# Performance work log

Hardware: AMD Instinct MI355X
Metric: run time of the kernel (lower is better)

## Reference

```python
import jax, jax.numpy as jnp
import numpy as np

B, D, UD = 32, 1024, 256          # batch, chunks_dim, units_dim
ENT, NENT = 32, 64                # entity_size, n_entities
S, C = NENT * ENT, NENT + 1       # src_len (units), n_chunks
NEG_INF = float('-inf')


def setup_inputs() -> dict:
    key = jax.random.key(0)
    ks = jax.random.split(key, 9)
    source = jax.random.normal(ks[0], (B, D), jnp.float32)
    high_level_repr = jax.random.normal(ks[1], (C, B, D), jnp.float32)
    pos_embs = jax.random.normal(ks[2], (S, B, UD), jnp.float32)
    low_level_repr = jax.random.normal(ks[3], (S, B, D), jnp.float32)
    low_level_mask = jax.random.randint(ks[4], (NENT, B, ENT), 0, 2).astype(bool)
    high_level_mask = jax.random.randint(ks[5], (1, B, C), 0, 2).astype(bool)
    high_level_mask = high_level_mask.at[..., 0].set(False)  # avoid all-masked chunk softmax
    W_unit = jax.random.normal(ks[6], (UD, D), jnp.float32) / np.sqrt(D)
    W_chunk = jax.random.normal(ks[7], (D, D), jnp.float32) / np.sqrt(D)
    W_out = jax.random.normal(ks[8], (D, 2 * D), jnp.float32) / np.sqrt(2 * D)
    return {"source": source, "high_level_repr": high_level_repr, "pos_embs": pos_embs,
            "low_level_repr": low_level_repr, "low_level_mask": low_level_mask,
            "high_level_mask": high_level_mask, "W_unit": W_unit, "W_chunk": W_chunk,
            "W_out": W_out}


def reference(source, high_level_repr, pos_embs, low_level_repr,
              low_level_mask, high_level_mask, W_unit, W_chunk, W_out):
    # batch-first views (torch transposes(0,1))
    hl = jnp.swapaxes(high_level_repr, 0, 1)    # (B, C, D)
    ll = jnp.swapaxes(low_level_repr, 0, 1)     # (B, S, D)
    pe = jnp.swapaxes(pos_embs, 0, 1)           # (B, S, UD)
    ll_mask = jnp.swapaxes(low_level_mask, 0, 1)   # (B, NENT, ENT)
    hl_mask = jnp.swapaxes(high_level_mask, 0, 1)  # (B, 1, C)

    # 'general' attention scorers, tgt_len == 1
    q_u = source @ W_unit.T                      # (B, UD)
    align_units = jnp.einsum('bd,bsd->bs', q_u, pe)        # (B, S)
    q_c = source @ W_chunk.T                     # (B, D)
    align_chunks = jnp.einsum('bd,bcd->bc', q_c, hl)[:, None, :]  # (B, 1, C)

    # low-level masked softmax per entity, NaN rows -> 0
    au = align_units.reshape(B, NENT, ENT)
    au = jnp.where(ll_mask, NEG_INF, au)
    au = jax.nn.softmax(au, axis=-1)
    all_masked = jnp.all(ll_mask, axis=-1)       # (B, NENT) rows that were NaN
    au = jnp.where(all_masked[..., None], 0.0, au)
    au = au.reshape(B, 1, S)

    # high-level masked softmax, drop chunk 0, inflate to unit granularity
    ac = jnp.where(hl_mask, NEG_INF, align_chunks)
    ac = jax.nn.softmax(ac, axis=-1)[:, :, 1:]   # (B, 1, C-1)
    ac_inflated = jnp.repeat(ac, ENT, axis=-1)   # (B, 1, S)

    align_vectors = ac_inflated * au             # (B, 1, S)
    c = jnp.einsum('bts,bsd->btd', align_vectors, ll)  # (B, 1, D)
    concat = jnp.concatenate([c, source[:, None, :]], axis=-1).reshape(B, 2 * D)
    attn_h = jnp.tanh(concat @ W_out.T)          # (B, D); tanh since attn_type='general'

    return (attn_h,
            align_vectors[:, 0, :],              # (B, S)
            ac[:, 0, :],                         # (B, C-1)
            au.reshape(B, S))                    # (B, S)
```

## Files before the change

### kernel.cpp

```cpp
#include <hip/hip_runtime.h>

#define B 32
#define D 1024
#define UD 256
#define ENT 32
#define NENT 64
#define S 2048
#define C 65

__device__ __forceinline__ float dot4(float4 w, const float* q) {
    return w.x * q[0] + w.y * q[1] + w.z * q[2] + w.w * q[3];
}

__global__ __launch_bounds__(256) void k_proj(const float* __restrict__ src,
                                              const float* __restrict__ Wu,
                                              const float* __restrict__ Wc,
                                              float* __restrict__ qu,
                                              float* __restrict__ qc) {
    __shared__ alignas(16) float s_src[4][D];
    __shared__ float red[4][64][4];
    int t = threadIdx.x, rg = blockIdx.x, bg = blockIdx.y;
    for (int f = t; f < 4 * (D / 4); f += 256) {
        int bb = f >> 8, i4 = f & 255;
        float4 v = *(const float4*)(src + (size_t)(bg * 4 + bb) * D + i4 * 4);
        *(float4*)(&s_src[bb][i4 * 4]) = v;
    }
    __syncthreads();
    int jl = t & 63, kq = t >> 6;
    int gj = rg * 64 + jl;
    const float* wrow = (gj < UD) ? (Wu + (size_t)gj * D) : (Wc + (size_t)(gj - UD) * D);
    const float4* wp = (const float4*)wrow + kq * 64;
    float acc[4] = {0.f, 0.f, 0.f, 0.f};
#pragma unroll 4
    for (int i = 0; i < 64; ++i) {
        float4 w = wp[i];
        int k = kq * 256 + i * 4;
#pragma unroll
        for (int bb = 0; bb < 4; ++bb) acc[bb] += dot4(w, &s_src[bb][k]);
    }
#pragma unroll
    for (int bb = 0; bb < 4; ++bb) red[kq][jl][bb] = acc[bb];
    __syncthreads();
    {
        int jl2 = t & 63, bb = t >> 6;
        float s = red[0][jl2][bb] + red[1][jl2][bb] + red[2][jl2][bb] + red[3][jl2][bb];
        int gj2 = rg * 64 + jl2, b = bg * 4 + bb;
        if (gj2 < UD) qu[b * UD + gj2] = s;
        else qc[b * D + (gj2 - UD)] = s;
    }
}

__global__ __launch_bounds__(256) void k_units(const float* __restrict__ pe,
                                               const int* __restrict__ lmask,
                                               const float* __restrict__ qu,
                                               float* __restrict__ out_au) {
    __shared__ alignas(16) float q[UD];
    __shared__ float part[256];
    int n = blockIdx.x, b = blockIdx.y, t = threadIdx.x;
    q[t] = qu[b * UD + t];
    __syncthreads();
    int e = t >> 3, r = t & 7;
    const float4* pp = (const float4*)(pe + (size_t)(n * ENT + e) * B * UD + (size_t)b * UD) + r * 8;
    float acc = 0.f;
#pragma unroll
    for (int i = 0; i < 8; ++i) acc += dot4(pp[i], &q[(r * 8 + i) * 4]);
    part[t] = acc;
    __syncthreads();
    if (t < ENT) {
        float sc = 0.f;
#pragma unroll
        for (int r2 = 0; r2 < 8; ++r2) sc += part[t * 8 + r2];
        bool m = lmask[(size_t)n * B * ENT + b * ENT + t] != 0;
        float v = m ? -1e30f : sc;
        float mx = v;
        for (int o = 16; o >= 1; o >>= 1) mx = fmaxf(mx, __shfl_xor(mx, o));
        float p = m ? 0.f : __expf(v - mx);
        float sm = p;
        for (int o = 16; o >= 1; o >>= 1) sm += __shfl_xor(sm, o);
        out_au[b * S + n * ENT + t] = (sm > 0.f) ? (p / sm) : 0.f;
    }
}

__global__ __launch_bounds__(256) void k_chunks(const float* __restrict__ hl,
                                                const int* __restrict__ hmask,
                                                const float* __restrict__ qc,
                                                float* __restrict__ out_ac) {
    __shared__ alignas(16) float q[D];
    __shared__ float sc[C];
    __shared__ float red[2];
    int b = blockIdx.x, t = threadIdx.x;
    for (int i = t; i < D / 4; i += 256)
        *(float4*)(&q[i * 4]) = *(const float4*)(qc + (size_t)b * D + i * 4);
    __syncthreads();
    int w = t >> 6, l = t & 63;
    for (int c = w; c < C; c += 4) {
        const float4* hp = (const float4*)(hl + (size_t)(c * B + b) * D);
        float acc = 0.f;
#pragma unroll
        for (int i = 0; i < 4; ++i) {
            int f = l + 64 * i;
            float4 h = hp[f];
            acc += dot4(h, &q[f * 4]);
        }
        for (int o = 32; o >= 1; o >>= 1) acc += __shfl_xor(acc, o);
        if (l == 0) sc[c] = acc;
    }
    __syncthreads();
    if (t == 0) {
        float mx = -1e30f;
        for (int c = 0; c < C; ++c) {
            float v = hmask[b * C + c] ? -1e30f : sc[c];
            mx = fmaxf(mx, v);
        }
        float sm = 0.f;
        for (int c = 0; c < C; ++c) {
            float v = hmask[b * C + c] ? -1e30f : sc[c];
            sm += __expf(v - mx);
        }
        red[0] = mx;
        red[1] = sm;
    }
    __syncthreads();
    if (t >= 1 && t < C) {
        bool m = hmask[b * C + t] != 0;
        float p = m ? 0.f : __expf(sc[t] - red[0]) / red[1];
        out_ac[b * NENT + (t - 1)] = p;
    }
}

__global__ __launch_bounds__(256) void k_ctx(const float* __restrict__ ll,
                                             const float* __restrict__ out_au,
                                             const float* __restrict__ out_ac,
                                             float* __restrict__ pf,
                                             float* __restrict__ out_av) {
    __shared__ float s_av[256];
    int ss = blockIdx.x, b = blockIdx.y, t = threadIdx.x;
    {
        int s = ss * 256 + t;
        int n = s >> 5;
        float a = out_ac[b * NENT + n] * out_au[b * S + s];
        s_av[t] = a;
        out_av[b * S + s] = a;
    }
    __syncthreads();
    float4 acc = {0.f, 0.f, 0.f, 0.f};
    const float4* base = (const float4*)(ll + (size_t)(ss * 256) * B * D + (size_t)b * D) + t;
#pragma unroll 8
    for (int j = 0; j < 256; ++j) {
        float4 x = base[(size_t)j * (B * D / 4)];
        float wv = s_av[j];
        acc.x += wv * x.x;
        acc.y += wv * x.y;
        acc.z += wv * x.z;
        acc.w += wv * x.w;
    }
    *(float4*)(pf + (size_t)ss * B * D + (size_t)b * D + t * 4) = acc;
}

__global__ __launch_bounds__(256) void k_red(const float* __restrict__ pf,
                                             float* __restrict__ cf) {
    int f = blockIdx.x * 256 + threadIdx.x;
    float s = 0.f;
#pragma unroll
    for (int ss = 0; ss < 8; ++ss) s += pf[(size_t)ss * B * D + f];
    cf[f] = s;
}

__global__ __launch_bounds__(256) void k_out(const float* __restrict__ Wo,
                                             const float* __restrict__ src,
                                             const float* __restrict__ cf,
                                             float* __restrict__ out_h) {
    __shared__ alignas(16) float cc[4][2 * D];
    __shared__ float red[4][64][4];
    int t = threadIdx.x, jg = blockIdx.x, bg = blockIdx.y;
    for (int f = t; f < 4 * (2 * D / 4); f += 256) {
        int bb = f >> 9, part = f & 511;
        int b = bg * 4 + bb;
        float4 v;
        if (part < 256) v = *(const float4*)(cf + (size_t)b * D + part * 4);
        else v = *(const float4*)(src + (size_t)b * D + (part - 256) * 4);
        *(float4*)(&cc[bb][part * 4]) = v;
    }
    __syncthreads();
    int jl = t & 63, kq = t >> 6;
    int j = jg * 64 + jl;
    const float4* wp = (const float4*)(Wo + (size_t)j * 2 * D) + kq * 128;
    float acc[4] = {0.f, 0.f, 0.f, 0.f};
#pragma unroll 4
    for (int i = 0; i < 128; ++i) {
        float4 w = wp[i];
        int k = kq * 512 + i * 4;
#pragma unroll
        for (int bb = 0; bb < 4; ++bb) acc[bb] += dot4(w, &cc[bb][k]);
    }
#pragma unroll
    for (int bb = 0; bb < 4; ++bb) red[kq][jl][bb] = acc[bb];
    __syncthreads();
    {
        int jl2 = t & 63, bb = t >> 6;
        float s = red[0][jl2][bb] + red[1][jl2][bb] + red[2][jl2][bb] + red[3][jl2][bb];
        out_h[(size_t)(bg * 4 + bb) * D + jg * 64 + jl2] = tanhf(s);
    }
}

extern "C" void kernel_launch(void* const* d_in, const int* in_sizes, int n_in,
                              void* d_out, int out_size, void* d_ws, size_t ws_size,
                              hipStream_t stream) {
    const float* src = (const float*)d_in[0];
    const float* hl = (const float*)d_in[1];
    const float* pe = (const float*)d_in[2];
    const float* ll = (const float*)d_in[3];
    const int* lmask = (const int*)d_in[4];
    const int* hmask = (const int*)d_in[5];
    const float* Wu = (const float*)d_in[6];
    const float* Wc = (const float*)d_in[7];
    const float* Wo = (const float*)d_in[8];

    float* out = (float*)d_out;
    float* out_h = out;
    float* out_av = out + B * D;
    float* out_ac = out_av + B * S;
    float* out_au = out_ac + B * NENT;

    float* ws = (float*)d_ws;
    float* qu = ws;
    float* qc = qu + B * UD;
    float* cf = qc + B * D;
    float* pf = cf + B * D;

    k_proj<<<dim3(20, 8), 256, 0, stream>>>(src, Wu, Wc, qu, qc);
    k_units<<<dim3(NENT, B), 256, 0, stream>>>(pe, lmask, qu, out_au);
    k_chunks<<<dim3(B), 256, 0, stream>>>(hl, hmask, qc, out_ac);
    k_ctx<<<dim3(8, B), 256, 0, stream>>>(ll, out_au, out_ac, pf, out_av);
    k_red<<<dim3(B * D / 256), 256, 0, stream>>>(pf, cf);
    k_out<<<dim3(16, 8), 256, 0, stream>>>(Wo, src, cf, out_h);
}
```

Before: 478.2 us.

## Fuse unit scoring, softmaxes and context reduction into one kernel; parallelize chunk scores

Chunk scores move into a new kernel with one block per (chunk, batch), which raises parallelism over the old 32-block chunk kernel. Unit scoring, the per-entity softmax, the chunk softmax and the weighted context sum now run in one 512-thread kernel per (slab, batch). Inside that kernel the context loop is split into two halves that are combined through shared memory. The separate slab-reduction kernel is dropped and its work folded into k_out's load phase. This removes launches and global round trips of intermediates, but the fused kernel still has only 256 blocks and each one recomputes the chunk softmax.

```diff
diff --git a/kernel.cpp b/kernel.cpp
--- a/kernel.cpp
+++ b/kernel.cpp
@@ -7,6 +7,8 @@
 #define NENT 64
 #define S 2048
 #define C 65
+#define NSLAB 8
+#define SROWS 256
 
 __device__ __forceinline__ float dot4(float4 w, const float* q) {
     return w.x * q[0] + w.y * q[1] + w.z * q[2] + w.w * q[3];
@@ -50,125 +52,121 @@
     }
 }
 
-__global__ __launch_bounds__(256) void k_units(const float* __restrict__ pe,
+__global__ __launch_bounds__(256) void k_score(const float* __restrict__ hl,
+                                               const float* __restrict__ qc,
+                                               float* __restrict__ sc) {
+    __shared__ float red[4];
+    int c = blockIdx.x, b = blockIdx.y, t = threadIdx.x;
+    const float4* hp = (const float4*)(hl + ((size_t)c * B + b) * D);
+    const float4* qp = (const float4*)(qc + (size_t)b * D);
+    float4 h = hp[t];
+    float4 q = qp[t];
+    float acc = h.x * q.x + h.y * q.y + h.z * q.z + h.w * q.w;
+    for (int o = 32; o >= 1; o >>= 1) acc += __shfl_xor(acc, o);
+    if ((t & 63) == 0) red[t >> 6] = acc;
+    __syncthreads();
+    if (t == 0) sc[b * C + c] = red[0] + red[1] + red[2] + red[3];
+}
+
+__global__ __launch_bounds__(512) void k_fused(const float* __restrict__ pe,
+                                               const float* __restrict__ ll,
                                                const int* __restrict__ lmask,
+                                               const int* __restrict__ hmask,
                                                const float* __restrict__ qu,
-                                               float* __restrict__ out_au) {
+                                               const float* __restrict__ sc,
+                                               float* __restrict__ pf,
+                                               float* __restrict__ out_au,
+                                               float* __restrict__ out_ac,
+                                               float* __restrict__ out_av) {
     __shared__ alignas(16) float q[UD];
-    __shared__ float part[256];
-    int n = blockIdx.x, b = blockIdx.y, t = threadIdx.x;
-    q[t] = qu[b * UD + t];
-    __syncthreads();
-    int e = t >> 3, r = t & 7;
-    const float4* pp = (const float4*)(pe + (size_t)(n * ENT + e) * B * UD + (size_t)b * UD) + r * 8;
-    float acc = 0.f;
-#pragma unroll
-    for (int i = 0; i < 8; ++i) acc += dot4(pp[i], &q[(r * 8 + i) * 4]);
-    part[t] = acc;
-    __syncthreads();
-    if (t < ENT) {
-        float sc = 0.f;
-#pragma unroll
-        for (int r2 = 0; r2 < 8; ++r2) sc += part[t * 8 + r2];
-        bool m = lmask[(size_t)n * B * ENT + b * ENT + t] != 0;
-        float v = m ? -1e30f : sc;
+    __shared__ float s_ac[NENT];
+    __shared__ float s_sc[SROWS];
+    __shared__ float s_av[SROWS];
+    __shared__ alignas(16) float4 s_red[256];
+    int ss = blockIdx.x, b = blockIdx.y, t = threadIdx.x;
+
+    if (t < UD) q[t] = qu[b * UD + t];
+
+    if (t < 64) {
+        bool m1 = hmask[b * C + t] != 0;
+        float x1 = m1 ? -1e30f : sc[b * C + t];
+        float x2 = -1e30f;
+        bool m2 = true;
+        if (t == 0) { m2 = hmask[b * C + 64] != 0; x2 = m2 ? -1e30f : sc[b * C + 64]; }
+        float mx = fmaxf(x1, x2);
+        for (int o = 32; o >= 1; o >>= 1) mx = fmaxf(mx, __shfl_xor(mx, o));
+        float e1 = m1 ? 0.f : __expf(x1 - mx);
+        float sm = e1 + ((t == 0 && !m2) ? __expf(x2 - mx) : 0.f);
+        for (int o = 32; o >= 1; o >>= 1) sm += __shfl_xor(sm, o);
+        bool mc = hmask[b * C + (t + 1)] != 0;
+        float xc = mc ? 0.f : sc[b * C + (t + 1)];
+        float p = mc ? 0.f : __expf(xc - mx) / sm;
+        s_ac[t] = p;
+        if (ss == 0) out_ac[b * NENT + t] = p;
+    }
+    __syncthreads();
+
+    int rg = t >> 3, r = t & 7;
+#pragma unroll
+    for (int pass = 0; pass < 4; ++pass) {
+        int j = pass * 64 + rg;
+        int s = ss * SROWS + j;
+        const float4* pp = (const float4*)(pe + ((size_t)s * B + b) * UD) + r;
+        float acc = 0.f;
+#pragma unroll
+        for (int i = 0; i < 8; ++i) {
+            float4 v = pp[i * 8];
+            acc += dot4(v, &q[(r + i * 8) * 4]);
+        }
+        for (int o = 1; o < 8; o <<= 1) acc += __shfl_xor(acc, o);
+        if (r == 0) s_sc[j] = acc;
+    }
+    __syncthreads();
+
+    if (t < SROWS) {
+        int j = t, e = j & 31;
+        int n = ss * 8 + (j >> 5);
+        bool m = lmask[((size_t)n * B + b) * ENT + e] != 0;
+        float v = m ? -1e30f : s_sc[j];
         float mx = v;
         for (int o = 16; o >= 1; o >>= 1) mx = fmaxf(mx, __shfl_xor(mx, o));
         float p = m ? 0.f : __expf(v - mx);
         float sm = p;
         for (int o = 16; o >= 1; o >>= 1) sm += __shfl_xor(sm, o);
-        out_au[b * S + n * ENT + t] = (sm > 0.f) ? (p / sm) : 0.f;
-    }
-}
-
-__global__ __launch_bounds__(256) void k_chunks(const float* __restrict__ hl,
-                                                const int* __restrict__ hmask,
-                                                const float* __restrict__ qc,
-                                                float* __restrict__ out_ac) {
-    __shared__ alignas(16) float q[D];
-    __shared__ float sc[C];
-    __shared__ float red[2];
-    int b = blockIdx.x, t = threadIdx.x;
-    for (int i = t; i < D / 4; i += 256)
-        *(float4*)(&q[i * 4]) = *(const float4*)(qc + (size_t)b * D + i * 4);
-    __syncthreads();
-    int w = t >> 6, l = t & 63;
-    for (int c = w; c < C; c += 4) {
-        const float4* hp = (const float4*)(hl + (size_t)(c * B + b) * D);
-        float acc = 0.f;
-#pragma unroll
-        for (int i = 0; i < 4; ++i) {
-            int f = l + 64 * i;
-            float4 h = hp[f];
-            acc += dot4(h, &q[f * 4]);
-        }
-        for (int o = 32; o >= 1; o >>= 1) acc += __shfl_xor(acc, o);
-        if (l == 0) sc[c] = acc;
-    }
-    __syncthreads();
-    if (t == 0) {
-        float mx = -1e30f;
-        for (int c = 0; c < C; ++c) {
-            float v = hmask[b * C + c] ? -1e30f : sc[c];
-            mx = fmaxf(mx, v);
-        }
-        float sm = 0.f;
-        for (int c = 0; c < C; ++c) {
-            float v = hmask[b * C + c] ? -1e30f : sc[c];
-            sm += __expf(v - mx);
-        }
-        red[0] = mx;
-        red[1] = sm;
-    }
-    __syncthreads();
-    if (t >= 1 && t < C) {
-        bool m = hmask[b * C + t] != 0;
-        float p = m ? 0.f : __expf(sc[t] - red[0]) / red[1];
-        out_ac[b * NENT + (t - 1)] = p;
-    }
-}
-
-__global__ __launch_bounds__(256) void k_ctx(const float* __restrict__ ll,
-                                             const float* __restrict__ out_au,
-                                             const float* __restrict__ out_ac,
-                                             float* __restrict__ pf,
-                                             float* __restrict__ out_av) {
-    __shared__ float s_av[256];
-    int ss = blockIdx.x, b = blockIdx.y, t = threadIdx.x;
-    {
-        int s = ss * 256 + t;
-        int n = s >> 5;
-        float a = out_ac[b * NENT + n] * out_au[b * S + s];
-        s_av[t] = a;
-        out_av[b * S + s] = a;
-    }
-    __syncthreads();
+        float au = (sm > 0.f) ? p / sm : 0.f;
+        float av = s_ac[n] * au;
+        s_av[j] = av;
+        int s = ss * SROWS + j;
+        out_au[b * S + s] = au;
+        out_av[b * S + s] = av;
+    }
+    __syncthreads();
+
+    int half = t >> 8, tt = t & 255;
     float4 acc = {0.f, 0.f, 0.f, 0.f};
-    const float4* base = (const float4*)(ll + (size_t)(ss * 256) * B * D + (size_t)b * D) + t;
+    const float4* base =
+        (const float4*)(ll + ((size_t)(ss * SROWS + half * 128) * B + b) * D) + tt;
 #pragma unroll 8
-    for (int j = 0; j < 256; ++j) {
+    for (int j = 0; j < 128; ++j) {
         float4 x = base[(size_t)j * (B * D / 4)];
-        float wv = s_av[j];
-        acc.x += wv * x.x;
-        acc.y += wv * x.y;
-        acc.z += wv * x.z;
-        acc.w += wv * x.w;
-    }
-    *(float4*)(pf + (size_t)ss * B * D + (size_t)b * D + t * 4) = acc;
-}
-
-__global__ __launch_bounds__(256) void k_red(const float* __restrict__ pf,
-                                             float* __restrict__ cf) {
-    int f = blockIdx.x * 256 + threadIdx.x;
-    float s = 0.f;
-#pragma unroll
-    for (int ss = 0; ss < 8; ++ss) s += pf[(size_t)ss * B * D + f];
-    cf[f] = s;
+        float w = s_av[half * 128 + j];
+        acc.x += w * x.x;
+        acc.y += w * x.y;
+        acc.z += w * x.z;
+        acc.w += w * x.w;
+    }
+    if (half == 1) s_red[tt] = acc;
+    __syncthreads();
+    if (half == 0) {
+        float4 o = s_red[tt];
+        acc.x += o.x; acc.y += o.y; acc.z += o.z; acc.w += o.w;
+        *(float4*)(pf + ((size_t)ss * B + b) * D + tt * 4) = acc;
+    }
 }
 
 __global__ __launch_bounds__(256) void k_out(const float* __restrict__ Wo,
                                              const float* __restrict__ src,
-                                             const float* __restrict__ cf,
+                                             const float* __restrict__ pf,
                                              float* __restrict__ out_h) {
     __shared__ alignas(16) float cc[4][2 * D];
     __shared__ float red[4][64][4];
@@ -177,8 +175,18 @@
         int bb = f >> 9, part = f & 511;
         int b = bg * 4 + bb;
         float4 v;
-        if (part < 256) v = *(const float4*)(cf + (size_t)b * D + part * 4);
-        else v = *(const float4*)(src + (size_t)b * D + (part - 256) * 4);
+        if (part < 256) {
+            float4 a = {0.f, 0.f, 0.f, 0.f};
+            const float4* pp = (const float4*)(pf + (size_t)b * D) + part;
+#pragma unroll
+            for (int ssi = 0; ssi < NSLAB; ++ssi) {
+                float4 x = pp[(size_t)ssi * (B * D / 4)];
+                a.x += x.x; a.y += x.y; a.z += x.z; a.w += x.w;
+            }
+            v = a;
+        } else {
+            v = *(const float4*)(src + (size_t)b * D + (part - 256) * 4);
+        }
         *(float4*)(&cc[bb][part * 4]) = v;
     }
     __syncthreads();
@@ -225,13 +233,12 @@
     float* ws = (float*)d_ws;
     float* qu = ws;
     float* qc = qu + B * UD;
-    float* cf = qc + B * D;
-    float* pf = cf + B * D;
+    float* scb = qc + B * D;
+    float* pf = scb + B * C;
 
     k_proj<<<dim3(20, 8), 256, 0, stream>>>(src, Wu, Wc, qu, qc);
-    k_units<<<dim3(NENT, B), 256, 0, stream>>>(pe, lmask, qu, out_au);
-    k_chunks<<<dim3(B), 256, 0, stream>>>(hl, hmask, qc, out_ac);
-    k_ctx<<<dim3(8, B), 256, 0, stream>>>(ll, out_au, out_ac, pf, out_av);
-    k_red<<<dim3(B * D / 256), 256, 0, stream>>>(pf, cf);
-    k_out<<<dim3(16, 8), 256, 0, stream>>>(Wo, src, cf, out_h);
-}
+    k_score<<<dim3(C, B), 256, 0, stream>>>(hl, qc, scb);
+    k_fused<<<dim3(NSLAB, B), 512, 0, stream>>>(pe, ll, lmask, hmask, qu, scb,
+                                                pf, out_au, out_ac, out_av);
+    k_out<<<dim3(16, 8), 256, 0, stream>>>(Wo, src, pf, out_h);
+}
```

Result: faster. 461.8 us (-3.4%).
